# Performance work log

Hardware: AMD Instinct MI355X
Metric: run time of the kernel (lower is better)

The kernel has to match this reference:

```python
import jax, jax.numpy as jnp
import numpy as np

IN = 4096   # input_size * 2 (is_bichar)
H = 2048    # hidden_size
C = 4096    # number of lexicon inputs


def setup_inputs() -> dict:
    key = jax.random.key(0)
    ks = jax.random.split(key, 12)
    s = 0.02
    return {
        "x": jax.random.normal(ks[0], (1, IN), jnp.float32),
        "c_input": jax.random.normal(ks[1], (C, H), jnp.float32),
        "h0": jax.random.normal(ks[2], (1, H), jnp.float32),
        "c0": jax.random.normal(ks[3], (1, H), jnp.float32),
        "W_ih": jax.random.normal(ks[4], (4 * H, IN), jnp.float32) * s,
        "b_ih": jnp.zeros((4 * H,), jnp.float32),
        "W_hh": jax.random.normal(ks[5], (4 * H, H), jnp.float32) * s,
        "b_hh": jnp.zeros((4 * H,), jnp.float32),
        "aW_ih": jax.random.normal(ks[6], (H, IN), jnp.float32) * s,
        "ab_ih": jnp.zeros((H,), jnp.float32),
        "aW_hh": jax.random.normal(ks[7], (H, H), jnp.float32) * s,
        "ab_hh": jnp.zeros((H,), jnp.float32),
    }


def reference(x, c_input, h0, c0, W_ih, b_ih, W_hh, b_hh, aW_ih, ab_ih, aW_hh, ab_hh):
    # gate pre-activations: [1, 4H]
    lstm_vec = x @ W_ih.T + b_ih + h0 @ W_hh.T + b_hh
    i, f, o, g = jnp.split(lstm_vec, 4, axis=1)
    i = jax.nn.sigmoid(i)
    f = jax.nn.sigmoid(f + 1.0)  # computed but unused when lexicon is non-empty (faithful)
    g = jnp.tanh(g)
    o = jax.nn.sigmoid(o)
    # alpha over lexicon entries: [C, H] (x-projection broadcasts over C)
    alpha = jax.nn.sigmoid(x @ aW_ih.T + ab_ih + c_input @ aW_hh.T + ab_hh)
    # exp-normalize over the (C+1) candidates per hidden unit
    w = jnp.exp(jnp.concatenate([i, alpha], axis=0))  # [C+1, H]
    w = w / w.sum(axis=0)
    merge = jnp.concatenate([g, c_input], axis=0)  # [C+1, H]
    c1 = (merge * w).sum(axis=0, keepdims=True)  # [1, H]
    h1 = o * jnp.tanh(c1)
    return h1, c1
```

## Files before the change

### kernel.cpp

```cpp
#include <hip/hip_runtime.h>
#include <hip/hip_bf16.h>
#include <cstdint>

#define HDIM 2048
#define INDIM 4096
#define CDIM 4096
#define KDIM 2048

typedef __attribute__((ext_vector_type(4))) int int4v;

__device__ __forceinline__ void gload16(const void* g, void* l) {
  __builtin_amdgcn_global_load_lds(
      (const __attribute__((address_space(1))) void*)g,
      (__attribute__((address_space(3))) void*)l, 16, 0, 0);
}

#define LOADPIN() asm volatile("s_waitcnt vmcnt(0)" ::: "memory")

__global__ __launch_bounds__(256) void k_prep(
    const float* __restrict__ c_input, const float* __restrict__ aW_hh,
    int8_t* __restrict__ a8, int8_t* __restrict__ b8,
    float* __restrict__ dAs, float* __restrict__ dBs,
    const float* __restrict__ x, const float* __restrict__ h0,
    const float* __restrict__ aW_ih, const float* __restrict__ ab_ih,
    const float* __restrict__ ab_hh,
    const float* __restrict__ W_hh, const float* __restrict__ b_ih,
    const float* __restrict__ b_hh,
    float* __restrict__ xa2, float* __restrict__ gate_part,
    float* __restrict__ accz) {
  const int t = threadIdx.x;
  const int wid = t >> 6, lane = t & 63;

  if (blockIdx.x < 1536) {
    if (blockIdx.x == 0) {
#pragma unroll
      for (int i = 0; i < 16; ++i) accz[i * 256 + t] = 0.f;
    }
    const int row = blockIdx.x * 4 + wid;
    const float* src; int8_t* dst; float* dsc; int r;
    if (row < CDIM) { src = c_input; dst = a8; dsc = dAs; r = row; }
    else            { src = aW_hh;  dst = b8; dsc = dBs; r = row - CDIM; }
    const float4* s4 = (const float4*)(src + (size_t)r * KDIM);
    float4 v[8];
#pragma unroll
    for (int it = 0; it < 8; ++it) v[it] = s4[it * 64 + lane];
    LOADPIN();
    float am = 0.f;
#pragma unroll
    for (int it = 0; it < 8; ++it)
      am = fmaxf(am, fmaxf(fmaxf(fabsf(v[it].x), fabsf(v[it].y)),
                           fmaxf(fabsf(v[it].z), fabsf(v[it].w))));
#pragma unroll
    for (int off = 32; off > 0; off >>= 1) am = fmaxf(am, __shfl_xor(am, off));
    am = fmaxf(am, 1e-20f);
    const float inv = 127.0f / am;
    uint32_t* qd = (uint32_t*)(dst + (size_t)r * KDIM);
#pragma unroll
    for (int it = 0; it < 8; ++it) {
      uint32_t p = (uint32_t)(__float2int_rn(v[it].x * inv) & 0xFF)
                 | ((uint32_t)(__float2int_rn(v[it].y * inv) & 0xFF) << 8)
                 | ((uint32_t)(__float2int_rn(v[it].z * inv) & 0xFF) << 16)
                 | ((uint32_t)(__float2int_rn(v[it].w * inv) & 0xFF) << 24);
      qd[it * 64 + lane] = p;
    }
    if (lane == 0) dsc[r] = am * (1.0f / 127.0f);
    return;
  }

  if (blockIdx.x < 2048) {
    const int h = (blockIdx.x - 1536) * 4 + wid;
    const float4* x4 = (const float4*)x;
    const float4* wr4 = (const float4*)(aW_ih + (size_t)h * INDIM);
    float sum = 0.f;
#pragma unroll
    for (int g = 0; g < 2; ++g) {
      float4 w[8];
#pragma unroll
      for (int it = 0; it < 8; ++it) w[it] = wr4[(g * 8 + it) * 64 + lane];
      LOADPIN();
#pragma unroll
      for (int it = 0; it < 8; ++it) {
        float4 xv = x4[(g * 8 + it) * 64 + lane];
        sum += w[it].x * xv.x + w[it].y * xv.y + w[it].z * xv.z + w[it].w * xv.w;
      }
    }
#pragma unroll
    for (int off = 32; off > 0; off >>= 1) sum += __shfl_down(sum, off);
    if (lane == 0) xa2[h] = sum + ab_ih[h] + ab_hh[h];
    return;
  }

  const int vr = (blockIdx.x - 2048) * 4 + wid;
  const int typ = vr >> 11;
  const int h = vr & (HDIM - 1);
  const int grow = (typ == 0) ? h : (typ == 1) ? (2 * HDIM + h) : (3 * HDIM + h);
  const float4* wh4 = (const float4*)(W_hh + (size_t)grow * HDIM);
  const float4* h4 = (const float4*)h0;
  float sum = 0.f;
  {
    float4 w[8];
#pragma unroll
    for (int it = 0; it < 8; ++it) w[it] = wh4[it * 64 + lane];
    LOADPIN();
#pragma unroll
    for (int it = 0; it < 8; ++it) {
      float4 hv = h4[it * 64 + lane];
      sum += w[it].x * hv.x + w[it].y * hv.y + w[it].z * hv.z + w[it].w * hv.w;
    }
  }
#pragma unroll
  for (int off = 32; off > 0; off >>= 1) sum += __shfl_down(sum, off);
  if (lane == 0) gate_part[vr] = sum + b_ih[grow] + b_hh[grow];
}

__global__ __launch_bounds__(256, 4) void k_gemm_gemv(
    const int8_t* __restrict__ A, const int8_t* __restrict__ B,
    const float* __restrict__ dAs, const float* __restrict__ dBs,
    const float* __restrict__ c_in, const float* __restrict__ xa2,
    float* __restrict__ acc_se, float* __restrict__ acc_sce,
    const float* __restrict__ x, const float* __restrict__ W_ih,
    const float* __restrict__ gate_part,
    float* __restrict__ i_sig, float* __restrict__ o_sig,
    float* __restrict__ g_tanh) {
  __shared__ uint8_t As[2][8192];
  __shared__ uint8_t Bs[2][8192];
  const int t = threadIdx.x;
  const int lane = t & 63, wid = t >> 6;

  if (blockIdx.x < 512) {
    const int wr = wid >> 1, wc = wid & 1;
    const int l15 = lane & 15, l4 = lane >> 4;
    const int bid = blockIdx.x;
    const int bn = (bid & 7) * 2 + ((bid >> 3) & 1);
    const int bm = bid >> 4;
    const int m0 = bm * 128, n0 = bn * 128;

    int4v acc[4][4] = {};

    const int trow = t >> 2;
    const int tcol = (((t & 3) ^ ((trow >> 1) & 3)) * 16);
    const int8_t* Arow = A + (size_t)(m0 + trow) * KDIM + tcol;
    const int8_t* Brow = B + (size_t)(n0 + trow) * KDIM + tcol;

#define STAGE(buf, k0)                                                          \
    do {                                                                        \
      _Pragma("unroll")                                                         \
      for (int qq = 0; qq < 2; ++qq) {                                          \
        gload16(Arow + (size_t)qq * 64 * KDIM + (k0), As[buf] + qq * 4096 + t * 16); \
        gload16(Brow + (size_t)qq * 64 * KDIM + (k0), Bs[buf] + qq * 4096 + t * 16); \
      }                                                                         \
    } while (0)

    STAGE(0, 0);
    __syncthreads();

    int cur = 0;
    for (int ti = 0; ti < KDIM / 64; ++ti) {
      if (ti < KDIM / 64 - 1) STAGE(cur ^ 1, (ti + 1) * 64);
      int4v af[4], bfr[4];
#pragma unroll
      for (int m = 0; m < 4; ++m) {
        const int r = wr * 64 + m * 16 + l15;
        af[m] = *(const int4v*)(As[cur] + r * 64 + ((l4 ^ ((r >> 1) & 3)) * 16));
      }
#pragma unroll
      for (int n = 0; n < 4; ++n) {
        const int r = wc * 64 + n * 16 + l15;
        bfr[n] = *(const int4v*)(Bs[cur] + r * 64 + ((l4 ^ ((r >> 1) & 3)) * 16));
      }
#pragma unroll
      for (int m = 0; m < 4; ++m)
#pragma unroll
        for (int n = 0; n < 4; ++n)
          acc[m][n] = __builtin_amdgcn_mfma_i32_16x16x64_i8(af[m], bfr[n], acc[m][n], 0, 0, 0);
      __syncthreads();
      cur ^= 1;
    }
#undef STAGE

#pragma unroll
    for (int n = 0; n < 4; ++n) {
      const int hcol = n0 + wc * 64 + n * 16 + l15;
      const float xa = xa2[hcol];
      const float db = dBs[hcol];
      float se = 0.f, sce = 0.f;
#pragma unroll
      for (int m = 0; m < 4; ++m) {
        const int jbase = m0 + wr * 64 + m * 16 + l4 * 4;
#pragma unroll
        for (int rr = 0; rr < 4; ++rr) {
          const float sc = dAs[jbase + rr] * db;
          float z = (float)acc[m][n][rr] * sc + xa;
          float s = 1.f / (1.f + __expf(-z));
          float e = __expf(s);
          se += e;
          sce += c_in[(size_t)(jbase + rr) * HDIM + hcol] * e;
        }
      }
      se += __shfl_xor(se, 16); se += __shfl_xor(se, 32);
      sce += __shfl_xor(sce, 16); sce += __shfl_xor(sce, 32);
      if (l4 == 0) {
        atomicAdd(&acc_se[hcol], se);
        atomicAdd(&acc_sce[hcol], sce);
      }
    }
    return;
  }

  const int vr = (blockIdx.x - 512) * 4 + wid;
  const int typ = vr >> 11;
  const int h = vr & (HDIM - 1);
  const int grow = (typ == 0) ? h : (typ == 1) ? (2 * HDIM + h) : (3 * HDIM + h);
  const float4* x4 = (const float4*)x;
  const float4* wr4 = (const float4*)(W_ih + (size_t)grow * INDIM);
  float sum = 0.f;
  {
    float4 w[16];
#pragma unroll
    for (int it = 0; it < 16; ++it) w[it] = wr4[it * 64 + lane];
    LOADPIN();
#pragma unroll
    for (int it = 0; it < 16; ++it) {
      float4 xv = x4[it * 64 + lane];
      sum += w[it].x * xv.x + w[it].y * xv.y + w[it].z * xv.z + w[it].w * xv.w;
    }
  }
#pragma unroll
  for (int off = 32; off > 0; off >>= 1) sum += __shfl_down(sum, off);
  if (lane == 0) {
    float z = sum + gate_part[vr];
    if (typ == 0)      i_sig[h] = 1.f / (1.f + expf(-z));
    else if (typ == 1) o_sig[h] = 1.f / (1.f + expf(-z));
    else               g_tanh[h] = tanhf(z);
  }
}

__global__ __launch_bounds__(256) void k_final(
    const float* __restrict__ i_sig, const float* __restrict__ o_sig,
    const float* __restrict__ g_tanh, const float* __restrict__ acc_se,
    const float* __restrict__ acc_sce, float* __restrict__ out) {
  int h = blockIdx.x * 256 + threadIdx.x;
  if (h >= HDIM) return;
  float wi = expf(i_sig[h]);
  float tot = acc_se[h] + wi;
  float c1 = (acc_sce[h] + g_tanh[h] * wi) / tot;
  float h1 = o_sig[h] * tanhf(c1);
  out[h] = h1;
  out[HDIM + h] = c1;
}

extern "C" void kernel_launch(void* const* d_in, const int* in_sizes, int n_in,
                              void* d_out, int out_size, void* d_ws, size_t ws_size,
                              hipStream_t stream) {
  const float* x     = (const float*)d_in[0];
  const float* c_inp = (const float*)d_in[1];
  const float* h0    = (const float*)d_in[2];
  const float* W_ih  = (const float*)d_in[4];
  const float* b_ih  = (const float*)d_in[5];
  const float* W_hh  = (const float*)d_in[6];
  const float* b_hh  = (const float*)d_in[7];
  const float* aW_ih = (const float*)d_in[8];
  const float* ab_ih = (const float*)d_in[9];
  const float* aW_hh = (const float*)d_in[10];
  const float* ab_hh = (const float*)d_in[11];
  float* out = (float*)d_out;

  char* ws = (char*)d_ws;
  int8_t* a8 = (int8_t*)ws;
  int8_t* b8 = a8 + (size_t)CDIM * KDIM;
  float* dAs = (float*)(b8 + (size_t)HDIM * KDIM);
  float* dBs = dAs + CDIM;
  float* fb  = dBs + HDIM;
  float* i_sig    = fb;
  float* o_sig    = fb + HDIM;
  float* g_tanh   = fb + 2 * HDIM;
  float* xa2      = fb + 3 * HDIM;
  float* acc_se   = fb + 4 * HDIM;
  float* acc_sce  = fb + 5 * HDIM;
  float* gate_part = fb + 6 * HDIM;

  k_prep<<<3584, 256, 0, stream>>>(
      c_inp, aW_hh, a8, b8, dAs, dBs, x, h0, aW_ih, ab_ih, ab_hh,
      W_hh, b_ih, b_hh, xa2, gate_part, acc_se);
  k_gemm_gemv<<<512 + 1536, 256, 0, stream>>>(
      a8, b8, dAs, dBs, c_inp, xa2, acc_se, acc_sce,
      x, W_ih, gate_part, i_sig, o_sig, g_tanh);
  k_final<<<(HDIM + 255) / 256, 256, 0, stream>>>(i_sig, o_sig, g_tanh,
                                                  acc_se, acc_sce, out);
}
```

Before: 67.94 us.

## Co-schedule int8 GEMM and W_ih GEMV waves within the same workgroup

The GEMM blocks and the separate GEMV blocks become one 512-thread workgroup. Waves 0-3 run the int8 MFMA tile and waves 4-7 stream three W_ih gate rows (i, o, g) per hidden unit. The GEMV waves issue matching barriers so they can share the workgroup's s_barrier sequence with the GEMM waves. The GEMM loop now issues its next-stage global-to-LDS prefetch after the fragment reads and uses an explicit vmcnt wait plus a raw barrier. The aim is to overlap the memory-bound GEMV with the compute-bound GEMM on the same CU and cut block count, at the risk of barrier-count coupling and higher register and occupancy pressure from 512-thread blocks.

```diff
diff --git a/kernel.cpp b/kernel.cpp
--- a/kernel.cpp
+++ b/kernel.cpp
@@ -16,6 +16,16 @@
 }
 
 #define LOADPIN() asm volatile("s_waitcnt vmcnt(0)" ::: "memory")
+#define WGBAR()                                   \
+  do {                                            \
+    __builtin_amdgcn_sched_barrier(0);            \
+    __builtin_amdgcn_s_barrier();                 \
+    __builtin_amdgcn_sched_barrier(0);            \
+  } while (0)
+
+__device__ __forceinline__ float dot4(float4 a, float4 b) {
+  return a.x * b.x + a.y * b.y + a.z * b.z + a.w * b.w;
+}
 
 __global__ __launch_bounds__(256) void k_prep(
     const float* __restrict__ c_input, const float* __restrict__ aW_hh,
@@ -81,7 +91,7 @@
 #pragma unroll
       for (int it = 0; it < 8; ++it) {
         float4 xv = x4[(g * 8 + it) * 64 + lane];
-        sum += w[it].x * xv.x + w[it].y * xv.y + w[it].z * xv.z + w[it].w * xv.w;
+        sum += dot4(w[it], xv);
       }
     }
 #pragma unroll
@@ -103,17 +113,14 @@
     for (int it = 0; it < 8; ++it) w[it] = wh4[it * 64 + lane];
     LOADPIN();
 #pragma unroll
-    for (int it = 0; it < 8; ++it) {
-      float4 hv = h4[it * 64 + lane];
-      sum += w[it].x * hv.x + w[it].y * hv.y + w[it].z * hv.z + w[it].w * hv.w;
-    }
+    for (int it = 0; it < 8; ++it) sum += dot4(w[it], h4[it * 64 + lane]);
   }
 #pragma unroll
   for (int off = 32; off > 0; off >>= 1) sum += __shfl_down(sum, off);
   if (lane == 0) gate_part[vr] = sum + b_ih[grow] + b_hh[grow];
 }
 
-__global__ __launch_bounds__(256, 4) void k_gemm_gemv(
+__global__ __launch_bounds__(512, 4) void k_fused(
     const int8_t* __restrict__ A, const int8_t* __restrict__ B,
     const float* __restrict__ dAs, const float* __restrict__ dBs,
     const float* __restrict__ c_in, const float* __restrict__ xa2,
@@ -126,11 +133,11 @@
   __shared__ uint8_t Bs[2][8192];
   const int t = threadIdx.x;
   const int lane = t & 63, wid = t >> 6;
-
-  if (blockIdx.x < 512) {
+  const int bid = blockIdx.x;
+
+  if (wid < 4) {
     const int wr = wid >> 1, wc = wid & 1;
     const int l15 = lane & 15, l4 = lane >> 4;
-    const int bid = blockIdx.x;
     const int bn = (bid & 7) * 2 + ((bid >> 3) & 1);
     const int bm = bid >> 4;
     const int m0 = bm * 128, n0 = bn * 128;
@@ -152,11 +159,11 @@
     } while (0)
 
     STAGE(0, 0);
-    __syncthreads();
+    LOADPIN();
+    WGBAR();
 
     int cur = 0;
-    for (int ti = 0; ti < KDIM / 64; ++ti) {
-      if (ti < KDIM / 64 - 1) STAGE(cur ^ 1, (ti + 1) * 64);
+    for (int ti = 0; ti < 32; ++ti) {
       int4v af[4], bfr[4];
 #pragma unroll
       for (int m = 0; m < 4; ++m) {
@@ -168,12 +175,14 @@
         const int r = wc * 64 + n * 16 + l15;
         bfr[n] = *(const int4v*)(Bs[cur] + r * 64 + ((l4 ^ ((r >> 1) & 3)) * 16));
       }
+      if (ti < 31) STAGE(cur ^ 1, (ti + 1) * 64);
 #pragma unroll
       for (int m = 0; m < 4; ++m)
 #pragma unroll
         for (int n = 0; n < 4; ++n)
           acc[m][n] = __builtin_amdgcn_mfma_i32_16x16x64_i8(af[m], bfr[n], acc[m][n], 0, 0, 0);
-      __syncthreads();
+      LOADPIN();
+      WGBAR();
       cur ^= 1;
     }
 #undef STAGE
@@ -207,31 +216,54 @@
     return;
   }
 
-  const int vr = (blockIdx.x - 512) * 4 + wid;
-  const int typ = vr >> 11;
-  const int h = vr & (HDIM - 1);
-  const int grow = (typ == 0) ? h : (typ == 1) ? (2 * HDIM + h) : (3 * HDIM + h);
+  const int h = bid * 4 + (wid - 4);
+  const float4* WI = (const float4*)(W_ih + (size_t)h * INDIM);
+  const float4* WO = (const float4*)(W_ih + (size_t)(2 * HDIM + h) * INDIM);
+  const float4* WG = (const float4*)(W_ih + (size_t)(3 * HDIM + h) * INDIM);
   const float4* x4 = (const float4*)x;
-  const float4* wr4 = (const float4*)(W_ih + (size_t)grow * INDIM);
-  float sum = 0.f;
-  {
-    float4 w[16];
-#pragma unroll
-    for (int it = 0; it < 16; ++it) w[it] = wr4[it * 64 + lane];
-    LOADPIN();
-#pragma unroll
-    for (int it = 0; it < 16; ++it) {
-      float4 xv = x4[it * 64 + lane];
-      sum += w[it].x * xv.x + w[it].y * xv.y + w[it].z * xv.z + w[it].w * xv.w;
-    }
-  }
-#pragma unroll
-  for (int off = 32; off > 0; off >>= 1) sum += __shfl_down(sum, off);
+  float sI = 0.f, sO = 0.f, sG = 0.f;
+  float4 wI0, wI1, xv0, xv1, wO0, wO1, wG0, wG1;
+
+  wI0 = WI[lane]; xv0 = x4[lane];
+  WGBAR();
+  wO0 = WO[lane]; wG0 = WG[lane];
+  WGBAR();
+#pragma unroll
+  for (int c = 0; c < 15; ++c) {
+    if ((c & 1) == 0) {
+      wI1 = WI[(c + 1) * 64 + lane]; xv1 = x4[(c + 1) * 64 + lane];
+      sI += dot4(wI0, xv0);
+    } else {
+      wI0 = WI[(c + 1) * 64 + lane]; xv0 = x4[(c + 1) * 64 + lane];
+      sI += dot4(wI1, xv1);
+    }
+    WGBAR();
+    if ((c & 1) == 0) {
+      wO1 = WO[(c + 1) * 64 + lane]; wG1 = WG[(c + 1) * 64 + lane];
+      sO += dot4(wO0, xv0); sG += dot4(wG0, xv0);
+    } else {
+      wO0 = WO[(c + 1) * 64 + lane]; wG0 = WG[(c + 1) * 64 + lane];
+      sO += dot4(wO1, xv1); sG += dot4(wG1, xv1);
+    }
+    WGBAR();
+  }
+  sI += dot4(wI1, xv1);
+  WGBAR();
+  sO += dot4(wO1, xv1); sG += dot4(wG1, xv1);
+
+#pragma unroll
+  for (int off = 32; off > 0; off >>= 1) {
+    sI += __shfl_down(sI, off);
+    sO += __shfl_down(sO, off);
+    sG += __shfl_down(sG, off);
+  }
   if (lane == 0) {
-    float z = sum + gate_part[vr];
-    if (typ == 0)      i_sig[h] = 1.f / (1.f + expf(-z));
-    else if (typ == 1) o_sig[h] = 1.f / (1.f + expf(-z));
-    else               g_tanh[h] = tanhf(z);
+    float zI = sI + gate_part[h];
+    float zO = sO + gate_part[HDIM + h];
+    float zG = sG + gate_part[2 * HDIM + h];
+    i_sig[h] = 1.f / (1.f + expf(-zI));
+    o_sig[h] = 1.f / (1.f + expf(-zO));
+    g_tanh[h] = tanhf(zG);
   }
 }
 
@@ -282,7 +314,7 @@
   k_prep<<<3584, 256, 0, stream>>>(
       c_inp, aW_hh, a8, b8, dAs, dBs, x, h0, aW_ih, ab_ih, ab_hh,
       W_hh, b_ih, b_hh, xa2, gate_part, acc_se);
-  k_gemm_gemv<<<512 + 1536, 256, 0, stream>>>(
+  k_fused<<<512, 512, 0, stream>>>(
       a8, b8, dAs, dBs, c_inp, xa2, acc_se, acc_sce,
       x, W_ih, gate_part, i_sig, o_sig, g_tanh);
   k_final<<<(HDIM + 255) / 256, 256, 0, stream>>>(i_sig, o_sig, g_tanh,
```

Result: faster. 65.84 us (-3.1%).

## Move W_ih gate GEMV into streaming prep kernel and read int8 c_input in epilogue

Applied to the files above, without the earlier changes.

Moves the W_ih gate GEMV out of the int8 GEMM kernel and into the first streaming kernel, so the GEMM launch contains only MFMA tiles. The gate nonlinearities are now applied in the final kernel instead. The GEMM epilogue reads the already-quantized int8 c_input (scaled by dAs) instead of re-reading the fp32 c_input, which cuts epilogue traffic by 4x. The trade-off is extra quantization error in the weighted sum of c_input, and a longer first kernel that must stream W_ih as well.

```diff
diff --git a/kernel.cpp b/kernel.cpp
--- a/kernel.cpp
+++ b/kernel.cpp
@@ -17,26 +17,31 @@
 
 #define LOADPIN() asm volatile("s_waitcnt vmcnt(0)" ::: "memory")
 
-__global__ __launch_bounds__(256) void k_prep(
+__device__ __forceinline__ float dot4(float4 a, float4 b) {
+  return a.x * b.x + a.y * b.y + a.z * b.z + a.w * b.w;
+}
+
+__global__ __launch_bounds__(256) void k_stream(
     const float* __restrict__ c_input, const float* __restrict__ aW_hh,
     int8_t* __restrict__ a8, int8_t* __restrict__ b8,
     float* __restrict__ dAs, float* __restrict__ dBs,
     const float* __restrict__ x, const float* __restrict__ h0,
     const float* __restrict__ aW_ih, const float* __restrict__ ab_ih,
     const float* __restrict__ ab_hh,
-    const float* __restrict__ W_hh, const float* __restrict__ b_ih,
-    const float* __restrict__ b_hh,
-    float* __restrict__ xa2, float* __restrict__ gate_part,
-    float* __restrict__ accz) {
+    const float* __restrict__ W_ih, const float* __restrict__ W_hh,
+    const float* __restrict__ b_ih, const float* __restrict__ b_hh,
+    float* __restrict__ xa2, float* __restrict__ gp_hh,
+    float* __restrict__ gp_ih, float* __restrict__ accz) {
   const int t = threadIdx.x;
   const int wid = t >> 6, lane = t & 63;
-
-  if (blockIdx.x < 1536) {
-    if (blockIdx.x == 0) {
+  const int bid = blockIdx.x;
+
+  if (bid < 1536) {
+    if (bid == 0) {
 #pragma unroll
       for (int i = 0; i < 16; ++i) accz[i * 256 + t] = 0.f;
     }
-    const int row = blockIdx.x * 4 + wid;
+    const int row = bid * 4 + wid;
     const float* src; int8_t* dst; float* dsc; int r;
     if (row < CDIM) { src = c_input; dst = a8; dsc = dAs; r = row; }
     else            { src = aW_hh;  dst = b8; dsc = dBs; r = row - CDIM; }
@@ -67,8 +72,8 @@
     return;
   }
 
-  if (blockIdx.x < 2048) {
-    const int h = (blockIdx.x - 1536) * 4 + wid;
+  if (bid < 2048) {
+    const int h = (bid - 1536) * 4 + wid;
     const float4* x4 = (const float4*)x;
     const float4* wr4 = (const float4*)(aW_ih + (size_t)h * INDIM);
     float sum = 0.f;
@@ -79,10 +84,8 @@
       for (int it = 0; it < 8; ++it) w[it] = wr4[(g * 8 + it) * 64 + lane];
       LOADPIN();
 #pragma unroll
-      for (int it = 0; it < 8; ++it) {
-        float4 xv = x4[(g * 8 + it) * 64 + lane];
-        sum += w[it].x * xv.x + w[it].y * xv.y + w[it].z * xv.z + w[it].w * xv.w;
-      }
+      for (int it = 0; it < 8; ++it)
+        sum += dot4(w[it], x4[(g * 8 + it) * 64 + lane]);
     }
 #pragma unroll
     for (int off = 32; off > 0; off >>= 1) sum += __shfl_down(sum, off);
@@ -90,161 +93,153 @@
     return;
   }
 
-  const int vr = (blockIdx.x - 2048) * 4 + wid;
+  if (bid < 3584) {
+    const int vr = (bid - 2048) * 4 + wid;
+    const int typ = vr >> 11;
+    const int h = vr & (HDIM - 1);
+    const int grow = (typ == 0) ? h : (typ == 1) ? (2 * HDIM + h) : (3 * HDIM + h);
+    const float4* wh4 = (const float4*)(W_hh + (size_t)grow * HDIM);
+    const float4* h4 = (const float4*)h0;
+    float sum = 0.f;
+    {
+      float4 w[8];
+#pragma unroll
+      for (int it = 0; it < 8; ++it) w[it] = wh4[it * 64 + lane];
+      LOADPIN();
+#pragma unroll
+      for (int it = 0; it < 8; ++it) sum += dot4(w[it], h4[it * 64 + lane]);
+    }
+#pragma unroll
+    for (int off = 32; off > 0; off >>= 1) sum += __shfl_down(sum, off);
+    if (lane == 0) gp_hh[vr] = sum + b_ih[grow] + b_hh[grow];
+    return;
+  }
+
+  const int vr = (bid - 3584) * 4 + wid;
   const int typ = vr >> 11;
   const int h = vr & (HDIM - 1);
   const int grow = (typ == 0) ? h : (typ == 1) ? (2 * HDIM + h) : (3 * HDIM + h);
-  const float4* wh4 = (const float4*)(W_hh + (size_t)grow * HDIM);
-  const float4* h4 = (const float4*)h0;
+  const float4* wi4 = (const float4*)(W_ih + (size_t)grow * INDIM);
+  const float4* x4 = (const float4*)x;
   float sum = 0.f;
-  {
+#pragma unroll
+  for (int g = 0; g < 2; ++g) {
     float4 w[8];
 #pragma unroll
-    for (int it = 0; it < 8; ++it) w[it] = wh4[it * 64 + lane];
+    for (int it = 0; it < 8; ++it) w[it] = wi4[(g * 8 + it) * 64 + lane];
     LOADPIN();
 #pragma unroll
-    for (int it = 0; it < 8; ++it) {
-      float4 hv = h4[it * 64 + lane];
-      sum += w[it].x * hv.x + w[it].y * hv.y + w[it].z * hv.z + w[it].w * hv.w;
-    }
+    for (int it = 0; it < 8; ++it)
+      sum += dot4(w[it], x4[(g * 8 + it) * 64 + lane]);
   }
 #pragma unroll
   for (int off = 32; off > 0; off >>= 1) sum += __shfl_down(sum, off);
-  if (lane == 0) gate_part[vr] = sum + b_ih[grow] + b_hh[grow];
-}
-
-__global__ __launch_bounds__(256, 4) void k_gemm_gemv(
+  if (lane == 0) gp_ih[vr] = sum;
+}
+
+__global__ __launch_bounds__(256, 4) void k_gemm(
     const int8_t* __restrict__ A, const int8_t* __restrict__ B,
     const float* __restrict__ dAs, const float* __restrict__ dBs,
-    const float* __restrict__ c_in, const float* __restrict__ xa2,
-    float* __restrict__ acc_se, float* __restrict__ acc_sce,
-    const float* __restrict__ x, const float* __restrict__ W_ih,
-    const float* __restrict__ gate_part,
-    float* __restrict__ i_sig, float* __restrict__ o_sig,
-    float* __restrict__ g_tanh) {
+    const float* __restrict__ xa2,
+    float* __restrict__ acc_se, float* __restrict__ acc_sce) {
   __shared__ uint8_t As[2][8192];
   __shared__ uint8_t Bs[2][8192];
   const int t = threadIdx.x;
   const int lane = t & 63, wid = t >> 6;
-
-  if (blockIdx.x < 512) {
-    const int wr = wid >> 1, wc = wid & 1;
-    const int l15 = lane & 15, l4 = lane >> 4;
-    const int bid = blockIdx.x;
-    const int bn = (bid & 7) * 2 + ((bid >> 3) & 1);
-    const int bm = bid >> 4;
-    const int m0 = bm * 128, n0 = bn * 128;
-
-    int4v acc[4][4] = {};
-
-    const int trow = t >> 2;
-    const int tcol = (((t & 3) ^ ((trow >> 1) & 3)) * 16);
-    const int8_t* Arow = A + (size_t)(m0 + trow) * KDIM + tcol;
-    const int8_t* Brow = B + (size_t)(n0 + trow) * KDIM + tcol;
-
-#define STAGE(buf, k0)                                                          \
-    do {                                                                        \
-      _Pragma("unroll")                                                         \
-      for (int qq = 0; qq < 2; ++qq) {                                          \
-        gload16(Arow + (size_t)qq * 64 * KDIM + (k0), As[buf] + qq * 4096 + t * 16); \
-        gload16(Brow + (size_t)qq * 64 * KDIM + (k0), Bs[buf] + qq * 4096 + t * 16); \
-      }                                                                         \
-    } while (0)
-
-    STAGE(0, 0);
+  const int wr = wid >> 1, wc = wid & 1;
+  const int l15 = lane & 15, l4 = lane >> 4;
+  const int bid = blockIdx.x;
+  const int bn = (bid & 7) * 2 + ((bid >> 3) & 1);
+  const int bm = bid >> 4;
+  const int m0 = bm * 128, n0 = bn * 128;
+
+  int4v acc[4][4] = {};
+
+  const int trow = t >> 2;
+  const int tcol = (((t & 3) ^ ((trow >> 1) & 3)) * 16);
+  const int8_t* Arow = A + (size_t)(m0 + trow) * KDIM + tcol;
+  const int8_t* Brow = B + (size_t)(n0 + trow) * KDIM + tcol;
+
+#define STAGE(buf, k0)                                                        \
+  do {                                                                        \
+    _Pragma("unroll")                                                         \
+    for (int qq = 0; qq < 2; ++qq) {                                          \
+      gload16(Arow + (size_t)qq * 64 * KDIM + (k0), As[buf] + qq * 4096 + t * 16); \
+      gload16(Brow + (size_t)qq * 64 * KDIM + (k0), Bs[buf] + qq * 4096 + t * 16); \
+    }                                                                         \
+  } while (0)
+
+  STAGE(0, 0);
+  __syncthreads();
+
+  int cur = 0;
+  for (int ti = 0; ti < KDIM / 64; ++ti) {
+    if (ti < KDIM / 64 - 1) STAGE(cur ^ 1, (ti + 1) * 64);
+    int4v af[4], bfr[4];
+#pragma unroll
+    for (int m = 0; m < 4; ++m) {
+      const int r = wr * 64 + m * 16 + l15;
+      af[m] = *(const int4v*)(As[cur] + r * 64 + ((l4 ^ ((r >> 1) & 3)) * 16));
+    }
+#pragma unroll
+    for (int n = 0; n < 4; ++n) {
+      const int r = wc * 64 + n * 16 + l15;
+      bfr[n] = *(const int4v*)(Bs[cur] + r * 64 + ((l4 ^ ((r >> 1) & 3)) * 16));
+    }
+#pragma unroll
+    for (int m = 0; m < 4; ++m)
+#pragma unroll
+      for (int n = 0; n < 4; ++n)
+        acc[m][n] = __builtin_amdgcn_mfma_i32_16x16x64_i8(af[m], bfr[n], acc[m][n], 0, 0, 0);
     __syncthreads();
-
-    int cur = 0;
-    for (int ti = 0; ti < KDIM / 64; ++ti) {
-      if (ti < KDIM / 64 - 1) STAGE(cur ^ 1, (ti + 1) * 64);
-      int4v af[4], bfr[4];
-#pragma unroll
-      for (int m = 0; m < 4; ++m) {
-        const int r = wr * 64 + m * 16 + l15;
-        af[m] = *(const int4v*)(As[cur] + r * 64 + ((l4 ^ ((r >> 1) & 3)) * 16));
+    cur ^= 1;
+  }
+#undef STAGE
+
+#pragma unroll
+  for (int n = 0; n < 4; ++n) {
+    const int hcol = n0 + wc * 64 + n * 16 + l15;
+    const float xa = xa2[hcol];
+    const float db = dBs[hcol];
+    float se = 0.f, sce = 0.f;
+#pragma unroll
+    for (int m = 0; m < 4; ++m) {
+      const int jbase = m0 + wr * 64 + m * 16 + l4 * 4;
+#pragma unroll
+      for (int rr = 0; rr < 4; ++rr) {
+        const float da = dAs[jbase + rr];
+        float z = (float)acc[m][n][rr] * (da * db) + xa;
+        float s = 1.f / (1.f + __expf(-z));
+        float e = __expf(s);
+        se += e;
+        sce += (float)A[(size_t)(jbase + rr) * KDIM + hcol] * (da * e);
       }
-#pragma unroll
-      for (int n = 0; n < 4; ++n) {
-        const int r = wc * 64 + n * 16 + l15;
-        bfr[n] = *(const int4v*)(Bs[cur] + r * 64 + ((l4 ^ ((r >> 1) & 3)) * 16));
-      }
-#pragma unroll
-      for (int m = 0; m < 4; ++m)
-#pragma unroll
-        for (int n = 0; n < 4; ++n)
-          acc[m][n] = __builtin_amdgcn_mfma_i32_16x16x64_i8(af[m], bfr[n], acc[m][n], 0, 0, 0);
-      __syncthreads();
-      cur ^= 1;
-    }
-#undef STAGE
-
-#pragma unroll
-    for (int n = 0; n < 4; ++n) {
-      const int hcol = n0 + wc * 64 + n * 16 + l15;
-      const float xa = xa2[hcol];
-      const float db = dBs[hcol];
-      float se = 0.f, sce = 0.f;
-#pragma unroll
-      for (int m = 0; m < 4; ++m) {
-        const int jbase = m0 + wr * 64 + m * 16 + l4 * 4;
-#pragma unroll
-        for (int rr = 0; rr < 4; ++rr) {
-          const float sc = dAs[jbase + rr] * db;
-          float z = (float)acc[m][n][rr] * sc + xa;
-          float s = 1.f / (1.f + __expf(-z));
-          float e = __expf(s);
-          se += e;
-          sce += c_in[(size_t)(jbase + rr) * HDIM + hcol] * e;
-        }
-      }
-      se += __shfl_xor(se, 16); se += __shfl_xor(se, 32);
-      sce += __shfl_xor(sce, 16); sce += __shfl_xor(sce, 32);
-      if (l4 == 0) {
-        atomicAdd(&acc_se[hcol], se);
-        atomicAdd(&acc_sce[hcol], sce);
-      }
-    }
-    return;
-  }
-
-  const int vr = (blockIdx.x - 512) * 4 + wid;
-  const int typ = vr >> 11;
-  const int h = vr & (HDIM - 1);
-  const int grow = (typ == 0) ? h : (typ == 1) ? (2 * HDIM + h) : (3 * HDIM + h);
-  const float4* x4 = (const float4*)x;
-  const float4* wr4 = (const float4*)(W_ih + (size_t)grow * INDIM);
-  float sum = 0.f;
-  {
-    float4 w[16];
-#pragma unroll
-    for (int it = 0; it < 16; ++it) w[it] = wr4[it * 64 + lane];
-    LOADPIN();
-#pragma unroll
-    for (int it = 0; it < 16; ++it) {
-      float4 xv = x4[it * 64 + lane];
-      sum += w[it].x * xv.x + w[it].y * xv.y + w[it].z * xv.z + w[it].w * xv.w;
-    }
-  }
-#pragma unroll
-  for (int off = 32; off > 0; off >>= 1) sum += __shfl_down(sum, off);
-  if (lane == 0) {
-    float z = sum + gate_part[vr];
-    if (typ == 0)      i_sig[h] = 1.f / (1.f + expf(-z));
-    else if (typ == 1) o_sig[h] = 1.f / (1.f + expf(-z));
-    else               g_tanh[h] = tanhf(z);
+    }
+    se += __shfl_xor(se, 16); se += __shfl_xor(se, 32);
+    sce += __shfl_xor(sce, 16); sce += __shfl_xor(sce, 32);
+    if (l4 == 0) {
+      atomicAdd(&acc_se[hcol], se);
+      atomicAdd(&acc_sce[hcol], sce);
+    }
   }
 }
 
 __global__ __launch_bounds__(256) void k_final(
-    const float* __restrict__ i_sig, const float* __restrict__ o_sig,
-    const float* __restrict__ g_tanh, const float* __restrict__ acc_se,
-    const float* __restrict__ acc_sce, float* __restrict__ out) {
+    const float* __restrict__ gp_hh, const float* __restrict__ gp_ih,
+    const float* __restrict__ acc_se, const float* __restrict__ acc_sce,
+    float* __restrict__ out) {
   int h = blockIdx.x * 256 + threadIdx.x;
   if (h >= HDIM) return;
-  float wi = expf(i_sig[h]);
+  float zI = gp_hh[h] + gp_ih[h];
+  float zO = gp_hh[HDIM + h] + gp_ih[HDIM + h];
+  float zG = gp_hh[2 * HDIM + h] + gp_ih[2 * HDIM + h];
+  float i_sig = 1.f / (1.f + expf(-zI));
+  float o_sig = 1.f / (1.f + expf(-zO));
+  float g_tanh = tanhf(zG);
+  float wi = expf(i_sig);
   float tot = acc_se[h] + wi;
-  float c1 = (acc_sce[h] + g_tanh[h] * wi) / tot;
-  float h1 = o_sig[h] * tanhf(c1);
+  float c1 = (acc_sce[h] + g_tanh * wi) / tot;
+  float h1 = o_sig * tanhf(c1);
   out[h] = h1;
   out[HDIM + h] = c1;
 }
@@ -271,20 +266,16 @@
   float* dAs = (float*)(b8 + (size_t)HDIM * KDIM);
   float* dBs = dAs + CDIM;
   float* fb  = dBs + HDIM;
-  float* i_sig    = fb;
-  float* o_sig    = fb + HDIM;
-  float* g_tanh   = fb + 2 * HDIM;
-  float* xa2      = fb + 3 * HDIM;
-  float* acc_se   = fb + 4 * HDIM;
-  float* acc_sce  = fb + 5 * HDIM;
-  float* gate_part = fb + 6 * HDIM;
-
-  k_prep<<<3584, 256, 0, stream>>>(
+  float* xa2     = fb;
+  float* acc_se  = fb + HDIM;
+  float* acc_sce = fb + 2 * HDIM;
+  float* gp_hh   = fb + 3 * HDIM;
+  float* gp_ih   = fb + 6 * HDIM;
+
+  k_stream<<<5120, 256, 0, stream>>>(
       c_inp, aW_hh, a8, b8, dAs, dBs, x, h0, aW_ih, ab_ih, ab_hh,
-      W_hh, b_ih, b_hh, xa2, gate_part, acc_se);
-  k_gemm_gemv<<<512 + 1536, 256, 0, stream>>>(
-      a8, b8, dAs, dBs, c_inp, xa2, acc_se, acc_sce,
-      x, W_ih, gate_part, i_sig, o_sig, g_tanh);
-  k_final<<<(HDIM + 255) / 256, 256, 0, stream>>>(i_sig, o_sig, g_tanh,
+      W_ih, W_hh, b_ih, b_hh, xa2, gp_hh, gp_ih, acc_se);
+  k_gemm<<<512, 256, 0, stream>>>(a8, b8, dAs, dBs, xa2, acc_se, acc_sce);
+  k_final<<<(HDIM + 255) / 256, 256, 0, stream>>>(gp_hh, gp_ih,
                                                   acc_se, acc_sce, out);
 }
```

Result: slower. 73.87 us (+8.7%).
